# Kernel tuning notes

Hardware: AMD Instinct MI355X
Metric: run time of the kernel (lower is better)

Reference implementation:

```python
import jax, jax.numpy as jnp
import numpy as np

D_MODEL, D_FF, N_EXPERTS, TOP_K = 1024, 4096, 8, 2

def setup_inputs() -> dict:
    key = jax.random.key(0)
    k0, k1, k2, k3 = jax.random.split(key, 4)
    x = jax.random.normal(k0, (2, 2048, D_MODEL), dtype=jnp.float32)
    Wg = jax.random.normal(k1, (D_MODEL, N_EXPERTS), dtype=jnp.float32) * 0.02
    W1 = jax.random.normal(k2, (N_EXPERTS, D_MODEL, D_FF), dtype=jnp.float32) * 0.02
    b1 = jnp.zeros((N_EXPERTS, D_FF), dtype=jnp.float32)
    W2 = jax.random.normal(k3, (N_EXPERTS, D_FF, D_MODEL), dtype=jnp.float32) * 0.02
    b2 = jnp.zeros((N_EXPERTS, D_MODEL), dtype=jnp.float32)
    return {"x": x, "Wg": Wg, "W1": W1, "b1": b1, "W2": W2, "b2": b2}

def reference(x, Wg, W1, b1, W2, b2):
    B = x.shape[:-1]
    xs = x.reshape(-1, x.shape[-1])                 # [T, D]
    T = xs.shape[0]
    gate_logits = xs @ Wg                           # [T, E]
    weights, sel = jax.lax.top_k(gate_logits, TOP_K)  # [T, k]
    # softmax over the top-k logits, computed in fp32 then cast back (matches F.softmax(dtype=float).type_as)
    weights = jax.nn.softmax(weights.astype(jnp.float32), axis=1).astype(x.dtype)
    # dense all-experts MLP: [E, T, D_FF] -> [E, T, D]
    h = jax.nn.relu(jnp.einsum('td,edf->etf', xs, W1) + b1[:, None, :])
    out_e = jnp.einsum('etf,efd->etd', h, W2) + b2[:, None, :]
    # gather each token's top-k expert outputs and combine with routing weights
    tok = jnp.arange(T)
    picked = out_e[sel, tok[:, None]]               # [T, k, D]
    out = jnp.einsum('tk,tkd->td', weights, picked) # [T, D]
    return out.reshape(*B, x.shape[-1])
```

## Files before the change

### kernel.cpp

```cpp
#include <hip/hip_runtime.h>
#include <cstdint>
#include <cstddef>

#define T_TOKENS 4096
#define DM 1024
#define DF 4096
#define NE 8
#define TOPK 2
#define BK 32
#define MAX_MT 72
#define MSLOTS 8192

typedef short short8 __attribute__((ext_vector_type(8)));
typedef float f32x4 __attribute__((ext_vector_type(4)));

__device__ __forceinline__ unsigned short f2h_bits(float f) {
  _Float16 h = (_Float16)f;
  union { _Float16 h; unsigned short u; } v; v.h = h; return v.u;
}

typedef __attribute__((address_space(3))) void lds_void_t;
typedef __attribute__((address_space(1))) void gvoid_t;
__device__ __forceinline__ void gl_lds16(const void* g, void* l) {
  __builtin_amdgcn_global_load_lds((gvoid_t*)g, (lds_void_t*)l, 16, 0, 0);
}

__global__ void gate_kernel(const float* __restrict__ x, const float* __restrict__ Wg,
                            int* __restrict__ sel, float* __restrict__ wts,
                            int* __restrict__ counts, unsigned short* __restrict__ Xh) {
  int wave = threadIdx.x >> 6, lane = threadIdx.x & 63;
  int t = blockIdx.x * 4 + wave;
  const float* xr = x + (size_t)t * DM;
  unsigned short* xh = Xh + (size_t)t * DM;
  float acc[NE];
#pragma unroll
  for (int e = 0; e < NE; e++) acc[e] = 0.f;
#pragma unroll
  for (int j = 0; j < 4; j++) {
    int d4 = (lane + 64 * j) * 4;
    float4 v = *(const float4*)(xr + d4);
    ushort4 o;
    o.x = f2h_bits(v.x); o.y = f2h_bits(v.y); o.z = f2h_bits(v.z); o.w = f2h_bits(v.w);
    *(ushort4*)(xh + d4) = o;
    const float* wr = Wg + (size_t)d4 * NE;
#pragma unroll
    for (int e = 0; e < NE; e++) acc[e] += v.x * wr[e];
#pragma unroll
    for (int e = 0; e < NE; e++) acc[e] += v.y * wr[NE + e];
#pragma unroll
    for (int e = 0; e < NE; e++) acc[e] += v.z * wr[2 * NE + e];
#pragma unroll
    for (int e = 0; e < NE; e++) acc[e] += v.w * wr[3 * NE + e];
  }
#pragma unroll
  for (int e = 0; e < NE; e++) {
    float v = acc[e];
#pragma unroll
    for (int off = 32; off > 0; off >>= 1) v += __shfl_down(v, off, 64);
    acc[e] = v;
  }
  if (lane == 0) {
    int b0 = 0;
#pragma unroll
    for (int e = 1; e < NE; e++) if (acc[e] > acc[b0]) b0 = e;
    int b1 = (b0 == 0) ? 1 : 0;
#pragma unroll
    for (int e = 0; e < NE; e++) if (e != b0 && acc[e] > acc[b1]) b1 = e;
    float p = expf(acc[b1] - acc[b0]);
    float w0 = 1.f / (1.f + p);
    sel[t * 2] = b0; sel[t * 2 + 1] = b1;
    wts[t * 2] = w0; wts[t * 2 + 1] = p * w0;
    atomicAdd(&counts[b0], 1);
    atomicAdd(&counts[b1], 1);
  }
}

__global__ void scan_kernel(const int* __restrict__ counts, int* __restrict__ offsets,
                            int* __restrict__ tile_off, int* __restrict__ cursors) {
  if (threadIdx.x == 0) {
    int o = 0, to = 0;
    offsets[0] = 0; tile_off[0] = 0;
    for (int e = 0; e < NE; e++) {
      cursors[e] = o;
      o += counts[e];
      to += (counts[e] + 127) >> 7;
      offsets[e + 1] = o;
      tile_off[e + 1] = to;
    }
  }
}

__global__ void scatter_kernel(const int* __restrict__ sel, const float* __restrict__ wts,
                               int* __restrict__ cursors, int* __restrict__ rows,
                               float* __restrict__ rw, int* __restrict__ inv) {
  int t = blockIdx.x * 256 + threadIdx.x;
  if (t >= T_TOKENS) return;
#pragma unroll
  for (int k = 0; k < TOPK; k++) {
    int e = sel[t * 2 + k];
    int slot = atomicAdd(&cursors[e], 1);
    rows[slot] = t;
    rw[slot] = wts[t * 2 + k];
    inv[t * 2 + k] = slot;
  }
}

__global__ void transpose_convert(const float* __restrict__ W1, unsigned short* __restrict__ W1t,
                                  const float* __restrict__ W2, unsigned short* __restrict__ W2t) {
  __shared__ float tile[64 * 65];
  int z = blockIdx.y;
  int R, C;
  const float* inE;
  unsigned short* outE;
  int tidx = blockIdx.x;
  int bx, by;
  if (z < 8) {
    R = DM; C = DF;
    inE = W1 + (size_t)z * DM * DF;
    outE = W1t + (size_t)z * DM * DF;
    bx = tidx % (DF / 64); by = tidx / (DF / 64);
  } else {
    R = DF; C = DM;
    inE = W2 + (size_t)(z - 8) * DM * DF;
    outE = W2t + (size_t)(z - 8) * DM * DF;
    bx = tidx % (DM / 64); by = tidx / (DM / 64);
  }
  int c0 = bx * 64, r0 = by * 64;
  int tid = threadIdx.x;
  int rr = tid >> 4, c4 = (tid & 15) * 4;
#pragma unroll
  for (int it = 0; it < 4; it++) {
    int r = rr + 16 * it;
    float4 v = *(const float4*)(inE + (size_t)(r0 + r) * C + c0 + c4);
    tile[r * 65 + c4 + 0] = v.x;
    tile[r * 65 + c4 + 1] = v.y;
    tile[r * 65 + c4 + 2] = v.z;
    tile[r * 65 + c4 + 3] = v.w;
  }
  __syncthreads();
#pragma unroll
  for (int it = 0; it < 2; it++) {
    int idx = tid + 256 * it;
    int c = idx >> 3, r8 = (idx & 7) * 8;
    short8 val;
#pragma unroll
    for (int j = 0; j < 8; j++) val[j] = (short)f2h_bits(tile[(r8 + j) * 65 + c]);
    *(short8*)(outE + (size_t)(c0 + c) * R + r0 + r8) = val;
  }
}

template <int K, int N, int NT, int NSPLIT, bool INDIR, bool SECOND>
__global__ __launch_bounds__(256, 4) void moe_gemm(
    const unsigned short* __restrict__ Aall, const unsigned short* __restrict__ Ball,
    unsigned short* __restrict__ Hout, float* __restrict__ Sout,
    const float* __restrict__ bias, const int* __restrict__ counts,
    const int* __restrict__ offsets, const int* __restrict__ tile_off,
    const int* __restrict__ rows, const float* __restrict__ rw) {
  __shared__ __align__(16) unsigned short lds[16384];

  int id = blockIdx.x;
  int nt = id % NT;
  int rest = id / NT;
  int ks = rest % NSPLIT;
  int bx = rest / NSPLIT;
  int e = 0;
#pragma unroll 1
  while (e < NE && bx >= tile_off[e + 1]) e++;
  if (e >= NE) return;
  int lt = bx - tile_off[e];
  int cnt = counts[e];
  int m0 = lt * 128;
  int rowbase = offsets[e];
  int n0 = nt * 128;

  const int KS = K / NSPLIT;
  const int kbeg = ks * KS;

  const unsigned short* Be = Ball + ((size_t)e * N + n0) * K + kbeg;

  int tid = threadIdx.x;
  int lane = tid & 63, wave = tid >> 6;
  int wm = wave & 1, wn = wave >> 1;

  int rA0 = tid >> 2, rA1 = (256 + tid) >> 2;
  int segl = (tid & 3) ^ ((rA0 >> 1) & 3);
  int mA0 = m0 + rA0; if (mA0 >= cnt) mA0 = cnt - 1;
  int mA1 = m0 + rA1; if (mA1 >= cnt) mA1 = cnt - 1;
  size_t ia0 = INDIR ? (size_t)rows[rowbase + mA0] : (size_t)(rowbase + mA0);
  size_t ia1 = INDIR ? (size_t)rows[rowbase + mA1] : (size_t)(rowbase + mA1);
  const unsigned short* srcA0 = Aall + ia0 * K + kbeg + segl * 8;
  const unsigned short* srcA1 = Aall + ia1 * K + kbeg + segl * 8;
  const unsigned short* srcB0 = Be + (size_t)rA0 * K + segl * 8;
  const unsigned short* srcB1 = Be + (size_t)rA1 * K + segl * 8;

  int quad = lane >> 4, c15 = lane & 15;
  int sp = ((quad ^ ((c15 >> 1) & 3))) * 8;
  int aoff[4], boff[4];
#pragma unroll
  for (int t4 = 0; t4 < 4; t4++) {
    aoff[t4] = (wm * 64 + t4 * 16 + c15) * BK + sp;
    boff[t4] = (wn * 64 + t4 * 16 + c15) * BK + sp;
  }

  f32x4 acc[4][4] = {};

  auto stage = [&](int buf, int kk) {
    unsigned short* base = lds + (buf << 13);
    gl_lds16(srcA0 + kk, base + (size_t)tid * 8);
    gl_lds16(srcA1 + kk, base + (size_t)(256 + tid) * 8);
    gl_lds16(srcB0 + kk, base + 4096 + (size_t)tid * 8);
    gl_lds16(srcB1 + kk, base + 4096 + (size_t)(256 + tid) * 8);
  };
  auto compute = [&](int buf) {
    const unsigned short* bA = lds + (buf << 13);
    const unsigned short* bB = bA + 4096;
    short8 af[4], bfr[4];
#pragma unroll
    for (int t4 = 0; t4 < 4; t4++) {
      af[t4]  = *(const short8*)(bA + aoff[t4]);
      bfr[t4] = *(const short8*)(bB + boff[t4]);
    }
    __builtin_amdgcn_s_setprio(1);
#pragma unroll
    for (int tm = 0; tm < 4; tm++)
#pragma unroll
      for (int tn = 0; tn < 4; tn++)
        acc[tm][tn] = __builtin_amdgcn_mfma_f32_16x16x32_f16(af[tm], bfr[tn], acc[tm][tn], 0, 0, 0);
    __builtin_amdgcn_s_setprio(0);
  };

  const int NK = KS / BK;
  stage(0, 0);
  stage(1, BK);
#pragma unroll 1
  for (int it = 0; it < NK - 1; ++it) {
    asm volatile("s_waitcnt vmcnt(4)" ::: "memory");
    __builtin_amdgcn_s_barrier();
    compute(it & 1);
    asm volatile("s_waitcnt lgkmcnt(0)" ::: "memory");
    __builtin_amdgcn_sched_barrier(0);
    __builtin_amdgcn_s_barrier();
    if (it + 2 < NK) stage(it & 1, (it + 2) * BK);
  }
  asm volatile("s_waitcnt vmcnt(0)" ::: "memory");
  __builtin_amdgcn_s_barrier();
  compute((NK - 1) & 1);

  if constexpr (!SECOND) {
#pragma unroll 1
    for (int half = 0; half < 2; half++) {
      __syncthreads();
      if (wm == half) {
#pragma unroll
        for (int tm = 0; tm < 4; tm++) {
#pragma unroll
          for (int tn = 0; tn < 4; tn++) {
            int colL = wn * 64 + tn * 16 + c15;
            float b = bias[e * N + n0 + colL];
#pragma unroll
            for (int r = 0; r < 4; r++) {
              int rl = tm * 16 + quad * 4 + r;
              float v = fmaxf(acc[tm][tn][r] + b, 0.f);
              lds[rl * 136 + colL] = f2h_bits(v);
            }
          }
        }
      }
      __syncthreads();
#pragma unroll
      for (int i = 0; i < 4; i++) {
        int idx = tid + 256 * i;
        int row = idx >> 4, c8 = (idx & 15) * 8;
        int grow = m0 + half * 64 + row;
        if (grow < cnt) {
          short8 val = *(const short8*)(lds + row * 136 + c8);
          *(short8*)(Hout + (size_t)(rowbase + grow) * N + n0 + c8) = val;
        }
      }
    }
  } else {
    float* So = Sout + (size_t)ks * ((size_t)MSLOTS * N);
#pragma unroll
    for (int tm = 0; tm < 4; tm++) {
#pragma unroll
      for (int tn = 0; tn < 4; tn++) {
        int gcol = n0 + wn * 64 + tn * 16 + c15;
        float b = (ks == 0) ? bias[e * N + gcol] : 0.f;
#pragma unroll
        for (int r = 0; r < 4; r++) {
          int rl = wm * 64 + tm * 16 + quad * 4 + r;
          if (m0 + rl < cnt) {
            int slot = rowbase + m0 + rl;
            So[(size_t)slot * N + gcol] = (acc[tm][tn][r] + b) * rw[slot];
          }
        }
      }
    }
  }
}

__global__ void combine_kernel(const float* __restrict__ S, const int* __restrict__ inv,
                               float* __restrict__ out) {
  int wave = threadIdx.x >> 6, lane = threadIdx.x & 63;
  int t = blockIdx.x * 4 + wave;
  int s0 = inv[t * 2], s1 = inv[t * 2 + 1];
  const size_t HALF4 = (size_t)MSLOTS * DM / 4;
  const float4* a0 = (const float4*)S + (size_t)s0 * (DM / 4);
  const float4* a1 = a0 + HALF4;
  const float4* b0 = (const float4*)S + (size_t)s1 * (DM / 4);
  const float4* b1 = b0 + HALF4;
  float4* o = (float4*)(out + (size_t)t * DM);
#pragma unroll
  for (int j = 0; j < 4; j++) {
    int i = lane + 64 * j;
    float4 va = a0[i], vb = a1[i], vc = b0[i], vd = b1[i];
    float4 vo;
    vo.x = (va.x + vb.x) + (vc.x + vd.x);
    vo.y = (va.y + vb.y) + (vc.y + vd.y);
    vo.z = (va.z + vb.z) + (vc.z + vd.z);
    vo.w = (va.w + vb.w) + (vc.w + vd.w);
    o[i] = vo;
  }
}

extern "C" void kernel_launch(void* const* d_in, const int* in_sizes, int n_in,
                              void* d_out, int out_size, void* d_ws, size_t ws_size,
                              hipStream_t stream) {
  const float* x  = (const float*)d_in[0];
  const float* Wg = (const float*)d_in[1];
  const float* W1 = (const float*)d_in[2];
  const float* b1 = (const float*)d_in[3];
  const float* W2 = (const float*)d_in[4];
  const float* b2 = (const float*)d_in[5];
  float* out = (float*)d_out;

  char* ws = (char*)d_ws;
  int*   counts   = (int*)(ws + 0);
  int*   cursors  = (int*)(ws + 64);
  int*   offsets  = (int*)(ws + 128);
  int*   tile_off = (int*)(ws + 192);
  int*   sel      = (int*)(ws + 256);
  float* wts      = (float*)(ws + 33024);
  int*   rows     = (int*)(ws + 65792);
  float* rw       = (float*)(ws + 98560);
  int*   inv      = (int*)(ws + 131328);
  unsigned short* Xh  = (unsigned short*)(ws + 164096);
  unsigned short* H   = (unsigned short*)(ws + 8552704);
  unsigned short* W1t = (unsigned short*)(ws + 75661568);
  float*          S   = (float*)(ws + 75661568);
  unsigned short* W2t = (unsigned short*)(ws + 142770432);

  hipMemsetAsync(ws, 0, 128, stream);

  gate_kernel<<<T_TOKENS / 4, 256, 0, stream>>>(x, Wg, sel, wts, counts, Xh);
  scan_kernel<<<1, 64, 0, stream>>>(counts, offsets, tile_off, cursors);
  scatter_kernel<<<T_TOKENS / 256, 256, 0, stream>>>(sel, wts, cursors, rows, rw, inv);
  transpose_convert<<<dim3(1024, 16), 256, 0, stream>>>(W1, W1t, W2, W2t);

  moe_gemm<DM, DF, 32, 1, true, false><<<MAX_MT * 32, 256, 0, stream>>>(
      Xh, W1t, H, nullptr, b1, counts, offsets, tile_off, rows, rw);
  moe_gemm<DF, DM, 8, 2, false, true><<<MAX_MT * 8 * 2, 256, 0, stream>>>(
      H, W2t, nullptr, S, b2, counts, offsets, tile_off, rows, rw);

  combine_kernel<<<T_TOKENS / 4, 256, 0, stream>>>(S, inv, out);
}
```

Measured before the change: 677.1 us.

## Enlarge MoE GEMM tiles to 256x256 with 8-wave blocks and split-phase pipelining

Replaces the 128x128 tile, 4-wave GEMM with a 256x256 tile computed by 512 threads (8 waves, each holding 128x64 accumulators). K advances in 64-wide steps split into two 32-halves in a 128KB double-buffered LDS. A and B staging is interleaved with the two MFMA sub-phases. The aim is higher arithmetic intensity and fewer global loads per FLOP. In exchange it runs one block per CU, wastes more padding on each expert's tail tile, and launches fewer blocks, which may leave CUs idle.

```diff
diff --git a/kernel.cpp b/kernel.cpp
--- a/kernel.cpp
+++ b/kernel.cpp
@@ -7,8 +7,7 @@
 #define DF 4096
 #define NE 8
 #define TOPK 2
-#define BK 32
-#define MAX_MT 72
+#define MAX_MT 40
 #define MSLOTS 8192
 
 typedef short short8 __attribute__((ext_vector_type(8)));
@@ -83,7 +82,7 @@
     for (int e = 0; e < NE; e++) {
       cursors[e] = o;
       o += counts[e];
-      to += (counts[e] + 127) >> 7;
+      to += (counts[e] + 255) >> 8;
       offsets[e + 1] = o;
       tile_off[e + 1] = to;
     }
@@ -150,13 +149,13 @@
 }
 
 template <int K, int N, int NT, int NSPLIT, bool INDIR, bool SECOND>
-__global__ __launch_bounds__(256, 4) void moe_gemm(
+__global__ __launch_bounds__(512, 1) void moe_gemm(
     const unsigned short* __restrict__ Aall, const unsigned short* __restrict__ Ball,
     unsigned short* __restrict__ Hout, float* __restrict__ Sout,
     const float* __restrict__ bias, const int* __restrict__ counts,
     const int* __restrict__ offsets, const int* __restrict__ tile_off,
     const int* __restrict__ rows, const float* __restrict__ rw) {
-  __shared__ __align__(16) unsigned short lds[16384];
+  __shared__ __align__(16) unsigned short lds[65536];
 
   int id = blockIdx.x;
   int nt = id % NT;
@@ -169,129 +168,142 @@
   if (e >= NE) return;
   int lt = bx - tile_off[e];
   int cnt = counts[e];
-  int m0 = lt * 128;
+  int m0 = lt * 256;
   int rowbase = offsets[e];
-  int n0 = nt * 128;
+  int n0 = nt * 256;
 
   const int KS = K / NSPLIT;
+  const int NKT = KS / 64;
   const int kbeg = ks * KS;
-
-  const unsigned short* Be = Ball + ((size_t)e * N + n0) * K + kbeg;
 
   int tid = threadIdx.x;
   int lane = tid & 63, wave = tid >> 6;
-  int wm = wave & 1, wn = wave >> 1;
-
-  int rA0 = tid >> 2, rA1 = (256 + tid) >> 2;
-  int segl = (tid & 3) ^ ((rA0 >> 1) & 3);
-  int mA0 = m0 + rA0; if (mA0 >= cnt) mA0 = cnt - 1;
-  int mA1 = m0 + rA1; if (mA1 >= cnt) mA1 = cnt - 1;
-  size_t ia0 = INDIR ? (size_t)rows[rowbase + mA0] : (size_t)(rowbase + mA0);
-  size_t ia1 = INDIR ? (size_t)rows[rowbase + mA1] : (size_t)(rowbase + mA1);
-  const unsigned short* srcA0 = Aall + ia0 * K + kbeg + segl * 8;
-  const unsigned short* srcA1 = Aall + ia1 * K + kbeg + segl * 8;
-  const unsigned short* srcB0 = Be + (size_t)rA0 * K + segl * 8;
-  const unsigned short* srcB1 = Be + (size_t)rA1 * K + segl * 8;
-
+  int wm = wave >> 2, wn = wave & 3;
   int quad = lane >> 4, c15 = lane & 15;
-  int sp = ((quad ^ ((c15 >> 1) & 3))) * 8;
-  int aoff[4], boff[4];
-#pragma unroll
-  for (int t4 = 0; t4 < 4; t4++) {
-    aoff[t4] = (wm * 64 + t4 * 16 + c15) * BK + sp;
-    boff[t4] = (wn * 64 + t4 * 16 + c15) * BK + sp;
-  }
-
-  f32x4 acc[4][4] = {};
-
-  auto stage = [&](int buf, int kk) {
-    unsigned short* base = lds + (buf << 13);
-    gl_lds16(srcA0 + kk, base + (size_t)tid * 8);
-    gl_lds16(srcA1 + kk, base + (size_t)(256 + tid) * 8);
-    gl_lds16(srcB0 + kk, base + 4096 + (size_t)tid * 8);
-    gl_lds16(srcB1 + kk, base + 4096 + (size_t)(256 + tid) * 8);
+
+  int srow = tid >> 2;
+  int l8 = ((tid & 3) ^ (srow & 3)) * 8;
+  int ma0 = m0 + srow;        if (ma0 >= cnt) ma0 = cnt - 1;
+  int ma1 = m0 + 128 + srow;  if (ma1 >= cnt) ma1 = cnt - 1;
+  size_t ia0 = INDIR ? (size_t)rows[rowbase + ma0] : (size_t)(rowbase + ma0);
+  size_t ia1 = INDIR ? (size_t)rows[rowbase + ma1] : (size_t)(rowbase + ma1);
+  const unsigned short* pA0 = Aall + ia0 * K + kbeg + l8;
+  const unsigned short* pA1 = Aall + ia1 * K + kbeg + l8;
+  const unsigned short* pB0 = Ball + ((size_t)e * N + n0 + srow) * K + kbeg + l8;
+  const unsigned short* pB1 = pB0 + (size_t)128 * K;
+
+  int sp8 = (quad ^ (c15 & 3)) * 8;
+  int aBase = (wm * 128 + c15) * 32 + sp8;
+  int bBase = (wn * 64  + c15) * 32 + sp8 + 8192;
+
+  f32x4 acc[8][4] = {};
+
+  auto stageA = [&](int buf, int v, int h) {
+    unsigned short* b = lds + buf * 32768 + h * 16384;
+    int ko = v * 64 + h * 32;
+    gl_lds16(pA0 + ko, b + tid * 8);
+    gl_lds16(pA1 + ko, b + 4096 + tid * 8);
   };
-  auto compute = [&](int buf) {
-    const unsigned short* bA = lds + (buf << 13);
-    const unsigned short* bB = bA + 4096;
-    short8 af[4], bfr[4];
-#pragma unroll
-    for (int t4 = 0; t4 < 4; t4++) {
-      af[t4]  = *(const short8*)(bA + aoff[t4]);
-      bfr[t4] = *(const short8*)(bB + boff[t4]);
+  auto stageB = [&](int buf, int v, int h) {
+    unsigned short* b = lds + buf * 32768 + h * 16384 + 8192;
+    int ko = v * 64 + h * 32;
+    gl_lds16(pB0 + ko, b + tid * 8);
+    gl_lds16(pB1 + ko, b + 4096 + tid * 8);
+  };
+
+  stageA(0, 0, 0); stageB(0, 0, 0); stageA(0, 0, 1); stageB(0, 0, 1);
+
+#pragma unroll 1
+  for (int u = 0; u < NKT; ++u) {
+    int p = u & 1;
+    int v = (u + 1 < NKT) ? u + 1 : 0;
+#pragma unroll
+    for (int h = 0; h < 2; ++h) {
+      const unsigned short* L = lds + p * 32768 + h * 16384;
+      short8 bf[4], af[4];
+      stageA(p ^ 1, v, h);
+      asm volatile("s_waitcnt vmcnt(6)" ::: "memory");
+      __builtin_amdgcn_s_barrier();
+#pragma unroll
+      for (int n = 0; n < 4; ++n) bf[n] = *(const short8*)(L + bBase + n * 512);
+#pragma unroll
+      for (int m = 0; m < 4; ++m) af[m] = *(const short8*)(L + aBase + m * 512);
+      __builtin_amdgcn_s_setprio(1);
+#pragma unroll
+      for (int m = 0; m < 4; ++m)
+#pragma unroll
+        for (int n = 0; n < 4; ++n)
+          acc[m][n] = __builtin_amdgcn_mfma_f32_16x16x32_f16(af[m], bf[n], acc[m][n], 0, 0, 0);
+      __builtin_amdgcn_s_setprio(0);
+      asm volatile("s_waitcnt lgkmcnt(0)" ::: "memory");
+      __builtin_amdgcn_sched_barrier(0);
+      __builtin_amdgcn_s_barrier();
+      stageB(p ^ 1, v, h);
+      __builtin_amdgcn_s_barrier();
+#pragma unroll
+      for (int m = 0; m < 4; ++m) af[m] = *(const short8*)(L + aBase + (4 + m) * 512);
+      __builtin_amdgcn_s_setprio(1);
+#pragma unroll
+      for (int m = 0; m < 4; ++m)
+#pragma unroll
+        for (int n = 0; n < 4; ++n)
+          acc[4 + m][n] = __builtin_amdgcn_mfma_f32_16x16x32_f16(af[m], bf[n], acc[4 + m][n], 0, 0, 0);
+      __builtin_amdgcn_s_setprio(0);
+      asm volatile("s_waitcnt lgkmcnt(0)" ::: "memory");
+      __builtin_amdgcn_sched_barrier(0);
+      __builtin_amdgcn_s_barrier();
     }
-    __builtin_amdgcn_s_setprio(1);
-#pragma unroll
-    for (int tm = 0; tm < 4; tm++)
-#pragma unroll
-      for (int tn = 0; tn < 4; tn++)
-        acc[tm][tn] = __builtin_amdgcn_mfma_f32_16x16x32_f16(af[tm], bfr[tn], acc[tm][tn], 0, 0, 0);
-    __builtin_amdgcn_s_setprio(0);
-  };
-
-  const int NK = KS / BK;
-  stage(0, 0);
-  stage(1, BK);
-#pragma unroll 1
-  for (int it = 0; it < NK - 1; ++it) {
-    asm volatile("s_waitcnt vmcnt(4)" ::: "memory");
-    __builtin_amdgcn_s_barrier();
-    compute(it & 1);
-    asm volatile("s_waitcnt lgkmcnt(0)" ::: "memory");
-    __builtin_amdgcn_sched_barrier(0);
-    __builtin_amdgcn_s_barrier();
-    if (it + 2 < NK) stage(it & 1, (it + 2) * BK);
   }
   asm volatile("s_waitcnt vmcnt(0)" ::: "memory");
   __builtin_amdgcn_s_barrier();
-  compute((NK - 1) & 1);
 
   if constexpr (!SECOND) {
 #pragma unroll 1
-    for (int half = 0; half < 2; half++) {
-      __syncthreads();
-      if (wm == half) {
-#pragma unroll
-        for (int tm = 0; tm < 4; tm++) {
-#pragma unroll
-          for (int tn = 0; tn < 4; tn++) {
-            int colL = wn * 64 + tn * 16 + c15;
+    for (int q = 0; q < 4; ++q) {
+      if ((q >> 1) == wm) {
+        int mb = (q & 1) * 4;
+#pragma unroll
+        for (int m = 0; m < 4; ++m) {
+#pragma unroll
+          for (int n = 0; n < 4; ++n) {
+            int colL = wn * 64 + n * 16 + c15;
             float b = bias[e * N + n0 + colL];
 #pragma unroll
-            for (int r = 0; r < 4; r++) {
-              int rl = tm * 16 + quad * 4 + r;
-              float v = fmaxf(acc[tm][tn][r] + b, 0.f);
-              lds[rl * 136 + colL] = f2h_bits(v);
+            for (int r = 0; r < 4; ++r) {
+              int rl = m * 16 + quad * 4 + r;
+              float v = fmaxf(acc[mb + m][n][r] + b, 0.f);
+              lds[rl * 264 + colL] = f2h_bits(v);
             }
           }
         }
       }
       __syncthreads();
 #pragma unroll
-      for (int i = 0; i < 4; i++) {
-        int idx = tid + 256 * i;
-        int row = idx >> 4, c8 = (idx & 15) * 8;
-        int grow = m0 + half * 64 + row;
+      for (int i = 0; i < 4; ++i) {
+        int idx = tid + 512 * i;
+        int row = idx >> 5, c8 = (idx & 31) * 8;
+        int grow = m0 + q * 64 + row;
         if (grow < cnt) {
-          short8 val = *(const short8*)(lds + row * 136 + c8);
+          short8 val = *(const short8*)(lds + row * 264 + c8);
           *(short8*)(Hout + (size_t)(rowbase + grow) * N + n0 + c8) = val;
         }
       }
+      __syncthreads();
     }
   } else {
     float* So = Sout + (size_t)ks * ((size_t)MSLOTS * N);
 #pragma unroll
-    for (int tm = 0; tm < 4; tm++) {
-#pragma unroll
-      for (int tn = 0; tn < 4; tn++) {
-        int gcol = n0 + wn * 64 + tn * 16 + c15;
+    for (int m = 0; m < 8; ++m) {
+#pragma unroll
+      for (int n = 0; n < 4; ++n) {
+        int gcol = n0 + wn * 64 + n * 16 + c15;
         float b = (ks == 0) ? bias[e * N + gcol] : 0.f;
 #pragma unroll
-        for (int r = 0; r < 4; r++) {
-          int rl = wm * 64 + tm * 16 + quad * 4 + r;
+        for (int r = 0; r < 4; ++r) {
+          int rl = wm * 128 + m * 16 + quad * 4 + r;
           if (m0 + rl < cnt) {
             int slot = rowbase + m0 + rl;
-            So[(size_t)slot * N + gcol] = (acc[tm][tn][r] + b) * rw[slot];
+            So[(size_t)slot * N + gcol] = (acc[m][n][r] + b) * rw[slot];
           }
         }
       }
@@ -357,9 +369,9 @@
   scatter_kernel<<<T_TOKENS / 256, 256, 0, stream>>>(sel, wts, cursors, rows, rw, inv);
   transpose_convert<<<dim3(1024, 16), 256, 0, stream>>>(W1, W1t, W2, W2t);
 
-  moe_gemm<DM, DF, 32, 1, true, false><<<MAX_MT * 32, 256, 0, stream>>>(
+  moe_gemm<DM, DF, 16, 1, true, false><<<MAX_MT * 16, 512, 0, stream>>>(
       Xh, W1t, H, nullptr, b1, counts, offsets, tile_off, rows, rw);
-  moe_gemm<DF, DM, 8, 2, false, true><<<MAX_MT * 8 * 2, 256, 0, stream>>>(
+  moe_gemm<DF, DM, 4, 2, false, true><<<MAX_MT * 4 * 2, 512, 0, stream>>>(
       H, W2t, nullptr, S, b2, counts, offsets, tile_off, rows, rw);
 
   combine_kernel<<<T_TOKENS / 4, 256, 0, stream>>>(S, inv, out);
```

Measured after the change: 784.4 us. +15.9%, slower.
